# Optimization experiments

Measured on AMD Instinct MI355X. Metric: run time of the kernel, lower is better.

## Reference

```python
import jax, jax.numpy as jnp
import numpy as np

P = 7          # output_size
SCALE = 0.125  # spatial_scale
S = 2          # sampling_ratio


def setup_inputs() -> dict:
    key = jax.random.key(0)
    k1, k2, k3, k4, k5, k6 = jax.random.split(key, 6)
    N, C, H, W, R = 8, 256, 100, 100, 512
    x = jax.random.normal(k1, (N, C, H, W), dtype=jnp.float32)
    b = jax.random.randint(k2, (R,), 0, N).astype(jnp.float32)
    x1 = jax.random.uniform(k3, (R,)) * 600.0
    y1 = jax.random.uniform(k4, (R,)) * 600.0
    bw = 10.0 + jax.random.uniform(k5, (R,)) * 190.0
    bh = 10.0 + jax.random.uniform(k6, (R,)) * 190.0
    rois = jnp.stack([b, x1, y1, x1 + bw, y1 + bh], axis=1).astype(jnp.float32)
    return {"x": x, "rois": rois}


def _axis_terms(c, L):
    # Per-axis bilinear terms, matching torchvision bilinear_interpolate.
    valid = (c > -1.0) & (c < L)          # whole sample zeroed if out of range
    c = jnp.clip(c, 0.0, L - 1.0)          # low clamp at 0; >=L-1 -> frac 0
    lo = jnp.minimum(jnp.floor(c).astype(jnp.int32), L - 1)
    hi = jnp.minimum(lo + 1, L - 1)
    frac = c - lo.astype(c.dtype)
    w_lo = jnp.where(valid, 1.0 - frac, 0.0)
    w_hi = jnp.where(valid, frac, 0.0)
    return lo, hi, w_lo, w_hi


def roi_align(x, rois):
    # aligned=True RoIAlign. x: [N,C,H,W], rois: [R,5] -> [R,C,P,P]
    N, C, H, W = x.shape
    b = rois[:, 0].astype(jnp.int32)
    sx = rois[:, 1] * SCALE - 0.5
    sy = rois[:, 2] * SCALE - 0.5
    bin_w = (rois[:, 3] * SCALE - 0.5 - sx) / P
    bin_h = (rois[:, 4] * SCALE - 0.5 - sy) / P

    frac = (jnp.arange(S, dtype=x.dtype) + 0.5) / S   # sample offset within bin
    bins = jnp.arange(P, dtype=x.dtype)
    grid = bins[None, :, None] + frac[None, None, :]   # [1,P,S]
    ys = sy[:, None, None] + grid * bin_h[:, None, None]  # [R,P,S]
    xs = sx[:, None, None] + grid * bin_w[:, None, None]  # [R,P,S]

    yl, yh, wy1, wy2 = _axis_terms(ys, H)
    xl, xh, wx1, wx2 = _axis_terms(xs, W)

    bb = b[:, None, None, None, None]
    Yl, Yh = yl[:, :, :, None, None], yh[:, :, :, None, None]  # [R,P,S,1,1]
    Xl, Xh = xl[:, None, None, :, :], xh[:, None, None, :, :]  # [R,1,1,P,S]

    def g(Y, X):
        # gather -> [R,Py,Sy,Px,Sx,C]
        return x[bb, :, Y, X]

    def w(wy, wx):
        return (wy[:, :, :, None, None] * wx[:, None, None, :, :])[..., None]

    val = (g(Yl, Xl) * w(wy1, wx1) + g(Yl, Xh) * w(wy1, wx2)
           + g(Yh, Xl) * w(wy2, wx1) + g(Yh, Xh) * w(wy2, wx2))
    # average over the SxS sampling grid per bin
    out = val.sum(axis=(2, 4)) / float(S * S)   # [R,Py,Px,C]
    return jnp.transpose(out, (0, 3, 1, 2))      # [R,C,P,P]


def reference(x, rois):
    return roi_align(x, rois)
```

## Files before the change

### kernel.cpp

```cpp
#include <hip/hip_runtime.h>

#define POOL 7
#define CCH 256
#define HH 100
#define WW 100
#define HW (HH * WW)
#define MAXTH 28
#define NTAP 14
#define RECI 128
#define NT 256
#define ITEMS 2
#define SLOTF 896

static constexpr float SCALE = 0.125f;

__device__ __attribute__((aligned(16))) int g_rec[1024 * RECI];

__device__ __forceinline__ void tap_calc(float s0, float step, int k, int L,
                                         int& lo, int& hi, float& w1, float& w2)
{
    const int   p  = k >> 1, si = k & 1;
    const float g  = (float)p + ((float)si + 0.5f) * 0.5f;
    const float c  = s0 + g * step;
    const float Lf = (float)L;
    const bool  valid = (c > -1.0f) && (c < Lf);
    float cl = fminf(fmaxf(c, 0.0f), Lf - 1.0f);
    lo = (int)floorf(cl);
    if (lo > L - 1) lo = L - 1;
    hi = lo + 1;
    if (hi > L - 1) hi = L - 1;
    const float fr = cl - (float)lo;
    w1 = valid ? 1.0f - fr : 0.0f;
    w2 = valid ? fr : 0.0f;
}

__global__ __launch_bounds__(64) void roi_pre(const float* __restrict__ rois,
                                              int* __restrict__ rec, int R)
{
    const int r = blockIdx.x;
    if (r >= R) return;
    int* rr = (rec ? rec : g_rec) + r * RECI;
    const int t = threadIdx.x;

    const float sx0 = rois[r * 5 + 1] * SCALE - 0.5f;
    const float sy0 = rois[r * 5 + 2] * SCALE - 0.5f;
    const float bw  = (rois[r * 5 + 3] * SCALE - 0.5f - sx0) * (1.0f / POOL);
    const float bh  = (rois[r * 5 + 4] * SCALE - 0.5f - sy0) * (1.0f / POOL);

    if (t < 2 * NTAP) {
        const int   axis = (t >= NTAP) ? 1 : 0;
        const int   k    = axis ? t - NTAP : t;
        const float s0   = axis ? sy0 : sx0;
        const float st   = axis ? bh : bw;
        const int   L    = axis ? HH : WW;
        int lo, hi, lo0, u0; float w1, w2, ua, ub;
        tap_calc(s0, st, k, L, lo, hi, w1, w2);
        tap_calc(s0, st, 0, L, lo0, u0, ua, ub);
        const int base = axis ? lo0 : (lo0 & ~3);
        int* tp = rr + 8 + (axis ? 4 * NTAP : 0) + k * 4;
        tp[0] = max(lo - base, 0);
        tp[1] = max(hi - base, 0);
        tp[2] = __float_as_int(w1);
        tp[3] = __float_as_int(w2);
    } else if (t == 2 * NTAP) {
        int xl0, xh0, xl13, xh13, yl0, yh0, yl13, yh13; float a, b;
        tap_calc(sx0, bw, 0,        WW, xl0,  xh0,  a, b);
        tap_calc(sx0, bw, NTAP - 1, WW, xl13, xh13, a, b);
        tap_calc(sy0, bh, 0,        HH, yl0,  yh0,  a, b);
        tap_calc(sy0, bh, NTAP - 1, HH, yl13, yh13, a, b);
        const int xmin_al = xl0 & ~3;
        int TH  = yh13 - yl0 + 1; if (TH > MAXTH) TH = MAXTH;
        int nb4 = (xh13 - xmin_al) / 4 + 1;
        if (nb4 > 8) nb4 = 8;
        rr[0] = (int)rois[r * 5 + 0];
        rr[1] = xmin_al;
        rr[2] = yl0;
        rr[3] = TH;
        rr[4] = nb4;
        rr[5] = (65536 + nb4 - 1) / nb4;
    }
}

template <int NJ>
__device__ __forceinline__ void run2(
    const float* __restrict__ x, float* __restrict__ out,
    float* slot, const int* __restrict__ rr,
    int n, int c0, int r, int xmin_al, int ymin,
    int TWp, int tot, int magic, int nb4, int lane)
{
    const int bin = (lane < POOL * POOL) ? lane : POOL * POOL - 1;
    const int py  = bin / POOL;
    const int px  = bin - py * POOL;
    const int4* tp = (const int4*)(rr + 8);
    const int4 xt0 = tp[px * 2],        xt1 = tp[px * 2 + 1];
    const int4 yt0 = tp[NTAP + py * 2], yt1 = tp[NTAP + py * 2 + 1];
    __builtin_amdgcn_sched_barrier(0);

    const float* xa = x + ((size_t)(n * CCH + c0)) * HW
                        + (size_t)ymin * WW + xmin_al;
    const float* xb = xa + HW;

    #pragma unroll
    for (int j = 0; j < NJ; ++j) {
        const int idx = lane + 64 * j;
        const int row = (idx * magic) >> 16;
        const int b   = idx - row * nb4;
        const int go  = row * WW + (b << 2);
        float* la = slot + j * 256;
        float* lb = slot + SLOTF + j * 256;
        if (j < NJ - 1 || idx < tot) {
            __builtin_amdgcn_global_load_lds(
                (const __attribute__((address_space(1))) void*)(xa + go),
                (__attribute__((address_space(3))) void*)la, 16, 0, 0);
            __builtin_amdgcn_global_load_lds(
                (const __attribute__((address_space(1))) void*)(xb + go),
                (__attribute__((address_space(3))) void*)lb, 16, 0, 0);
        }
    }

    int   off[16];
    float wgt[16];
    {
        const int   rl0 = yt0.x * TWp, rh0 = yt0.y * TWp;
        const int   rl1 = yt1.x * TWp, rh1 = yt1.y * TWp;
        const float wy10 = __int_as_float(yt0.z), wy20 = __int_as_float(yt0.w);
        const float wy11 = __int_as_float(yt1.z), wy21 = __int_as_float(yt1.w);
        const float wx10 = __int_as_float(xt0.z), wx20 = __int_as_float(xt0.w);
        const float wx11 = __int_as_float(xt1.z), wx21 = __int_as_float(xt1.w);
        off[0]  = rl0 + xt0.x;  wgt[0]  = wy10 * wx10;
        off[1]  = rl0 + xt0.y;  wgt[1]  = wy10 * wx20;
        off[2]  = rh0 + xt0.x;  wgt[2]  = wy20 * wx10;
        off[3]  = rh0 + xt0.y;  wgt[3]  = wy20 * wx20;
        off[4]  = rl0 + xt1.x;  wgt[4]  = wy10 * wx11;
        off[5]  = rl0 + xt1.y;  wgt[5]  = wy10 * wx21;
        off[6]  = rh0 + xt1.x;  wgt[6]  = wy20 * wx11;
        off[7]  = rh0 + xt1.y;  wgt[7]  = wy20 * wx21;
        off[8]  = rl1 + xt0.x;  wgt[8]  = wy11 * wx10;
        off[9]  = rl1 + xt0.y;  wgt[9]  = wy11 * wx20;
        off[10] = rh1 + xt0.x;  wgt[10] = wy21 * wx10;
        off[11] = rh1 + xt0.y;  wgt[11] = wy21 * wx20;
        off[12] = rl1 + xt1.x;  wgt[12] = wy11 * wx11;
        off[13] = rl1 + xt1.y;  wgt[13] = wy11 * wx21;
        off[14] = rh1 + xt1.x;  wgt[14] = wy21 * wx11;
        off[15] = rh1 + xt1.y;  wgt[15] = wy21 * wx21;
    }

    asm volatile("s_waitcnt vmcnt(1)" ::: "memory");
    float a0 = 0.f, a1 = 0.f, a2 = 0.f, a3 = 0.f;
    #pragma unroll
    for (int i = 0; i < 16; i += 4) {
        a0 += wgt[i + 0] * slot[off[i + 0]];
        a1 += wgt[i + 1] * slot[off[i + 1]];
        a2 += wgt[i + 2] * slot[off[i + 2]];
        a3 += wgt[i + 3] * slot[off[i + 3]];
    }
    const float accA = (a0 + a1) + (a2 + a3);

    asm volatile("s_waitcnt vmcnt(0)" ::: "memory");
    const float* sb = slot + SLOTF;
    float b0 = 0.f, b1 = 0.f, b2 = 0.f, b3 = 0.f;
    #pragma unroll
    for (int i = 0; i < 16; i += 4) {
        b0 += wgt[i + 0] * sb[off[i + 0]];
        b1 += wgt[i + 1] * sb[off[i + 1]];
        b2 += wgt[i + 2] * sb[off[i + 2]];
        b3 += wgt[i + 3] * sb[off[i + 3]];
    }
    const float accB = (b0 + b1) + (b2 + b3);

    if (lane < POOL * POOL) {
        float* ob = out + ((size_t)(r * CCH + c0)) * (POOL * POOL) + bin;
        ob[0]           = accA * 0.25f;
        ob[POOL * POOL] = accB * 0.25f;
    }
}

__global__ __launch_bounds__(NT) void roi_main(
    const float* __restrict__ x, const int* __restrict__ rec_in,
    float* __restrict__ out)
{
    __shared__ float tile[(NT / 64) * ITEMS * SLOTF];

    const int bid  = blockIdx.x;
    const int r    = bid >> 5;
    const int g    = bid & 31;
    const int wid  = threadIdx.x >> 6;
    const int lane = threadIdx.x & 63;
    const int c0   = g * (ITEMS * NT / 64) + wid * ITEMS;

    const int* rr = (rec_in ? rec_in : g_rec) + r * RECI;
    const int4 ra = *(const int4*)rr;
    const int2 rb = *(const int2*)(rr + 4);
    const int n = ra.x, xmin_al = ra.y, ymin = ra.z, TH = ra.w;
    const int nb4 = rb.x, magic = rb.y;

    const int tot = TH * nb4;
    const int TWp = nb4 << 2;
    const int nj  = (tot + 63) >> 6;

    float* slot = tile + wid * (ITEMS * SLOTF);

    switch (nj) {
    case 1:  run2<1>(x, out, slot, rr, n, c0, r, xmin_al, ymin, TWp, tot, magic, nb4, lane); break;
    case 2:  run2<2>(x, out, slot, rr, n, c0, r, xmin_al, ymin, TWp, tot, magic, nb4, lane); break;
    case 3:  run2<3>(x, out, slot, rr, n, c0, r, xmin_al, ymin, TWp, tot, magic, nb4, lane); break;
    default: run2<4>(x, out, slot, rr, n, c0, r, xmin_al, ymin, TWp, tot, magic, nb4, lane); break;
    }
}

extern "C" void kernel_launch(void* const* d_in, const int* in_sizes, int n_in,
                              void* d_out, int out_size, void* d_ws, size_t ws_size,
                              hipStream_t stream) {
    const float* x    = (const float*)d_in[0];
    const float* rois = (const float*)d_in[1];
    float*       out  = (float*)d_out;

    const int R = in_sizes[1] / 5;
    int* rec = (ws_size >= (size_t)R * RECI * sizeof(int)) ? (int*)d_ws : nullptr;

    roi_pre<<<R, 64, 0, stream>>>(rois, rec, R);
    roi_main<<<R * 32, NT, 0, stream>>>(x, rec, out);
}
```

Before: 40.62 us.

## Fuse ROI precompute into main kernel and drop separate pre-pass launch

Removes the roi_pre kernel and its workspace record buffer. Each thread now computes the ROI bounds, tile extents and its own bilinear tap offsets and weights directly from the rois input. This saves a kernel launch and the dependency between the two kernels, at the cost of redundant per-thread arithmetic in every block. The magic divisor is now computed with a float ceil instead of integer division.

```diff
diff --git a/kernel.cpp b/kernel.cpp
--- a/kernel.cpp
+++ b/kernel.cpp
@@ -7,14 +7,11 @@
 #define HW (HH * WW)
 #define MAXTH 28
 #define NTAP 14
-#define RECI 128
 #define NT 256
 #define ITEMS 2
 #define SLOTF 896
 
 static constexpr float SCALE = 0.125f;
-
-__device__ __attribute__((aligned(16))) int g_rec[1024 * RECI];
 
 __device__ __forceinline__ void tap_calc(float s0, float step, int k, int L,
                                          int& lo, int& hi, float& w1, float& w2)
@@ -34,68 +31,14 @@
     w2 = valid ? fr : 0.0f;
 }
 
-__global__ __launch_bounds__(64) void roi_pre(const float* __restrict__ rois,
-                                              int* __restrict__ rec, int R)
-{
-    const int r = blockIdx.x;
-    if (r >= R) return;
-    int* rr = (rec ? rec : g_rec) + r * RECI;
-    const int t = threadIdx.x;
-
-    const float sx0 = rois[r * 5 + 1] * SCALE - 0.5f;
-    const float sy0 = rois[r * 5 + 2] * SCALE - 0.5f;
-    const float bw  = (rois[r * 5 + 3] * SCALE - 0.5f - sx0) * (1.0f / POOL);
-    const float bh  = (rois[r * 5 + 4] * SCALE - 0.5f - sy0) * (1.0f / POOL);
-
-    if (t < 2 * NTAP) {
-        const int   axis = (t >= NTAP) ? 1 : 0;
-        const int   k    = axis ? t - NTAP : t;
-        const float s0   = axis ? sy0 : sx0;
-        const float st   = axis ? bh : bw;
-        const int   L    = axis ? HH : WW;
-        int lo, hi, lo0, u0; float w1, w2, ua, ub;
-        tap_calc(s0, st, k, L, lo, hi, w1, w2);
-        tap_calc(s0, st, 0, L, lo0, u0, ua, ub);
-        const int base = axis ? lo0 : (lo0 & ~3);
-        int* tp = rr + 8 + (axis ? 4 * NTAP : 0) + k * 4;
-        tp[0] = max(lo - base, 0);
-        tp[1] = max(hi - base, 0);
-        tp[2] = __float_as_int(w1);
-        tp[3] = __float_as_int(w2);
-    } else if (t == 2 * NTAP) {
-        int xl0, xh0, xl13, xh13, yl0, yh0, yl13, yh13; float a, b;
-        tap_calc(sx0, bw, 0,        WW, xl0,  xh0,  a, b);
-        tap_calc(sx0, bw, NTAP - 1, WW, xl13, xh13, a, b);
-        tap_calc(sy0, bh, 0,        HH, yl0,  yh0,  a, b);
-        tap_calc(sy0, bh, NTAP - 1, HH, yl13, yh13, a, b);
-        const int xmin_al = xl0 & ~3;
-        int TH  = yh13 - yl0 + 1; if (TH > MAXTH) TH = MAXTH;
-        int nb4 = (xh13 - xmin_al) / 4 + 1;
-        if (nb4 > 8) nb4 = 8;
-        rr[0] = (int)rois[r * 5 + 0];
-        rr[1] = xmin_al;
-        rr[2] = yl0;
-        rr[3] = TH;
-        rr[4] = nb4;
-        rr[5] = (65536 + nb4 - 1) / nb4;
-    }
-}
-
 template <int NJ>
 __device__ __forceinline__ void run2(
     const float* __restrict__ x, float* __restrict__ out,
-    float* slot, const int* __restrict__ rr,
-    int n, int c0, int r, int xmin_al, int ymin,
-    int TWp, int tot, int magic, int nb4, int lane)
+    float* slot, int n, int c0, int r, int xmin_al, int ymin,
+    int TWp, int tot, int magic, int nb4, int lane,
+    const int4& xt0, const int4& xt1, const int4& yt0, const int4& yt1,
+    int bin)
 {
-    const int bin = (lane < POOL * POOL) ? lane : POOL * POOL - 1;
-    const int py  = bin / POOL;
-    const int px  = bin - py * POOL;
-    const int4* tp = (const int4*)(rr + 8);
-    const int4 xt0 = tp[px * 2],        xt1 = tp[px * 2 + 1];
-    const int4 yt0 = tp[NTAP + py * 2], yt1 = tp[NTAP + py * 2 + 1];
-    __builtin_amdgcn_sched_barrier(0);
-
     const float* xa = x + ((size_t)(n * CCH + c0)) * HW
                         + (size_t)ymin * WW + xmin_al;
     const float* xb = xa + HW;
@@ -176,7 +119,7 @@
 }
 
 __global__ __launch_bounds__(NT) void roi_main(
-    const float* __restrict__ x, const int* __restrict__ rec_in,
+    const float* __restrict__ x, const float* __restrict__ rois,
     float* __restrict__ out)
 {
     __shared__ float tile[(NT / 64) * ITEMS * SLOTF];
@@ -188,23 +131,55 @@
     const int lane = threadIdx.x & 63;
     const int c0   = g * (ITEMS * NT / 64) + wid * ITEMS;
 
-    const int* rr = (rec_in ? rec_in : g_rec) + r * RECI;
-    const int4 ra = *(const int4*)rr;
-    const int2 rb = *(const int2*)(rr + 4);
-    const int n = ra.x, xmin_al = ra.y, ymin = ra.z, TH = ra.w;
-    const int nb4 = rb.x, magic = rb.y;
+    const float r0  = rois[r * 5 + 0];
+    const float sx0 = rois[r * 5 + 1] * SCALE - 0.5f;
+    const float sy0 = rois[r * 5 + 2] * SCALE - 0.5f;
+    const float bw  = (rois[r * 5 + 3] * SCALE - 0.5f - sx0) * (1.0f / POOL);
+    const float bh  = (rois[r * 5 + 4] * SCALE - 0.5f - sy0) * (1.0f / POOL);
+    const int   n   = (int)r0;
 
-    const int tot = TH * nb4;
-    const int TWp = nb4 << 2;
-    const int nj  = (tot + 63) >> 6;
+    int xl0, xh0, xl13, xh13, yl0d, yh0d, yl13, yh13; float ua, ub;
+    tap_calc(sx0, bw, 0,        WW, xl0,  xh0,  ua, ub);
+    tap_calc(sx0, bw, NTAP - 1, WW, xl13, xh13, ua, ub);
+    tap_calc(sy0, bh, 0,        HH, yl0d, yh0d, ua, ub);
+    tap_calc(sy0, bh, NTAP - 1, HH, yl13, yh13, ua, ub);
+    const int xmin_al = xl0 & ~3;
+    const int ymin    = yl0d;
+    int TH  = yh13 - ymin + 1; if (TH > MAXTH) TH = MAXTH;
+    int nb4 = ((xh13 - xmin_al) >> 2) + 1;  if (nb4 > 8) nb4 = 8;
+    const int magic = (int)ceilf(65536.0f / (float)nb4);
+    const int tot   = TH * nb4;
+    const int TWp   = nb4 << 2;
+    const int nj    = (tot + 63) >> 6;
+
+    const int bin = (lane < POOL * POOL) ? lane : POOL * POOL - 1;
+    const int py  = bin / POOL;
+    const int px  = bin - py * POOL;
+
+    int4 xt0, xt1, yt0, yt1;
+    {
+        int lo, hi; float w1, w2;
+        tap_calc(sx0, bw, px * 2,     WW, lo, hi, w1, w2);
+        xt0 = make_int4(max(lo - xmin_al, 0), max(hi - xmin_al, 0),
+                        __float_as_int(w1), __float_as_int(w2));
+        tap_calc(sx0, bw, px * 2 + 1, WW, lo, hi, w1, w2);
+        xt1 = make_int4(max(lo - xmin_al, 0), max(hi - xmin_al, 0),
+                        __float_as_int(w1), __float_as_int(w2));
+        tap_calc(sy0, bh, py * 2,     HH, lo, hi, w1, w2);
+        yt0 = make_int4(max(lo - ymin, 0), max(hi - ymin, 0),
+                        __float_as_int(w1), __float_as_int(w2));
+        tap_calc(sy0, bh, py * 2 + 1, HH, lo, hi, w1, w2);
+        yt1 = make_int4(max(lo - ymin, 0), max(hi - ymin, 0),
+                        __float_as_int(w1), __float_as_int(w2));
+    }
 
     float* slot = tile + wid * (ITEMS * SLOTF);
 
     switch (nj) {
-    case 1:  run2<1>(x, out, slot, rr, n, c0, r, xmin_al, ymin, TWp, tot, magic, nb4, lane); break;
-    case 2:  run2<2>(x, out, slot, rr, n, c0, r, xmin_al, ymin, TWp, tot, magic, nb4, lane); break;
-    case 3:  run2<3>(x, out, slot, rr, n, c0, r, xmin_al, ymin, TWp, tot, magic, nb4, lane); break;
-    default: run2<4>(x, out, slot, rr, n, c0, r, xmin_al, ymin, TWp, tot, magic, nb4, lane); break;
+    case 1:  run2<1>(x, out, slot, n, c0, r, xmin_al, ymin, TWp, tot, magic, nb4, lane, xt0, xt1, yt0, yt1, bin); break;
+    case 2:  run2<2>(x, out, slot, n, c0, r, xmin_al, ymin, TWp, tot, magic, nb4, lane, xt0, xt1, yt0, yt1, bin); break;
+    case 3:  run2<3>(x, out, slot, n, c0, r, xmin_al, ymin, TWp, tot, magic, nb4, lane, xt0, xt1, yt0, yt1, bin); break;
+    default: run2<4>(x, out, slot, n, c0, r, xmin_al, ymin, TWp, tot, magic, nb4, lane, xt0, xt1, yt0, yt1, bin); break;
     }
 }
 
@@ -216,8 +191,5 @@
     float*       out  = (float*)d_out;
 
     const int R = in_sizes[1] / 5;
-    int* rec = (ws_size >= (size_t)R * RECI * sizeof(int)) ? (int*)d_ws : nullptr;
-
-    roi_pre<<<R, 64, 0, stream>>>(rois, rec, R);
-    roi_main<<<R * 32, NT, 0, stream>>>(x, rec, out);
+    roi_main<<<R * 32, NT, 0, stream>>>(x, rois, out);
 }
```

Result: faster. 36.53 us (-10.1%).
